# Kernel tuning notes

Measured on AMD Instinct MI355X. Metric: run time of the kernel, lower is better.

Reference implementation:

```python
import jax, jax.numpy as jnp
import numpy as np

D_MODEL = 1024
BATCH = 16
SEQ = 1024
RATIO = 2.0 / 3.0  # layer_idx=2, n_layers=4
THRESH = 0.5


def _layer_norm(x, gamma, beta, eps=1e-5):
    mu = jnp.mean(x, axis=-1, keepdims=True)
    var = jnp.var(x, axis=-1, keepdims=True)
    return (x - mu) * jax.lax.rsqrt(var + eps) * gamma + beta


def _ternary(x):
    # FixedThresholdTernarySpike(threshold=0.5): sign(x) if |x|>0.5 else 0
    return jnp.where(x > THRESH, 1.0, jnp.where(x < -THRESH, -1.0, 0.0)).astype(x.dtype)


def setup_inputs() -> dict:
    key = jax.random.key(0)
    ks = jax.random.split(key, 10)
    scale = 0.1 / np.sqrt(D_MODEL)
    x = jax.random.normal(ks[0], (BATCH, SEQ, D_MODEL), dtype=jnp.float32)
    S0 = jnp.zeros((BATCH, D_MODEL), dtype=jnp.float32)
    mix_init = 1.0 - RATIO
    return {
        "x": x,
        "S0": S0,
        "ln_gamma": jnp.ones((D_MODEL,), jnp.float32),
        "ln_beta": jnp.zeros((D_MODEL,), jnp.float32),
        "time_mix_k": jnp.full((D_MODEL,), mix_init, jnp.float32) + 0.02 * jax.random.normal(ks[1], (D_MODEL,)),
        "time_mix_v": jnp.full((D_MODEL,), mix_init, jnp.float32) + 0.02 * jax.random.normal(ks[2], (D_MODEL,)),
        "time_mix_r": jnp.full((D_MODEL,), mix_init, jnp.float32) + 0.02 * jax.random.normal(ks[3], (D_MODEL,)),
        "decay_weight": jnp.full((D_MODEL,), -0.5, jnp.float32) + 0.02 * jax.random.normal(ks[4], (D_MODEL,)),
        "Wk": scale * jax.random.normal(ks[5], (D_MODEL, D_MODEL), jnp.float32),
        "Wv": scale * jax.random.normal(ks[6], (D_MODEL, D_MODEL), jnp.float32),
        "Wr": scale * jax.random.normal(ks[7], (D_MODEL, D_MODEL), jnp.float32),
        "Wo": scale * jax.random.normal(ks[8], (D_MODEL, D_MODEL), jnp.float32),
    }


def reference(x, S0, ln_gamma, ln_beta, time_mix_k, time_mix_v, time_mix_r,
              decay_weight, Wk, Wv, Wr, Wo):
    # x: (B, T, D)
    x_norm = _layer_norm(x, ln_gamma, ln_beta)                       # LN applied to every step
    # prev_x at t is LN(x[t-1]); at t=0 it is zeros (module uses zeros_like, not LN of zeros)
    prev_norm = jnp.concatenate([jnp.zeros_like(x_norm[:, :1]), x_norm[:, :-1]], axis=1)

    xk = x_norm * time_mix_k + prev_norm * (1.0 - time_mix_k)
    xv = x_norm * time_mix_v + prev_norm * (1.0 - time_mix_v)
    xr = x_norm * time_mix_r + prev_norm * (1.0 - time_mix_r)

    k = _ternary(jnp.einsum('btd,ed->bte', xk, Wk))                  # ternary spikes
    v = _ternary(jnp.einsum('btd,ed->bte', xv, Wv))
    r = jax.nn.sigmoid(jnp.einsum('btd,ed->bte', xr, Wr))

    decay = jax.nn.sigmoid(decay_weight)                             # (D,)
    kv = k * v                                                       # (B, T, D)

    def step(S, kv_t):                                               # S: (B, D)
        S_new = decay * S + kv_t
        return S_new, S_new

    S_final, S_all = jax.lax.scan(step, S0, jnp.swapaxes(kv, 0, 1))  # S_all: (T, B, D)
    S_all = jnp.swapaxes(S_all, 0, 1)                                # (B, T, D)

    out = x + r * jnp.einsum('btd,ed->bte', S_all, Wo)
    return out, S_final
```

## Files before the change

kernel.cpp:

```cpp
#include <hip/hip_runtime.h>
#include <hip/hip_bf16.h>
#include <math.h>

#define D_MODEL 1024
#define SEQ 1024
#define BATCH 16
#define NROWS (BATCH * SEQ)
#define KT8 8

typedef float f32x4 __attribute__((ext_vector_type(4)));
typedef int   i32x4 __attribute__((ext_vector_type(4)));
typedef int   i32x8 __attribute__((ext_vector_type(8)));
typedef __hip_bfloat16 bf16;
typedef unsigned char u8;

__device__ __forceinline__ float bf2f(bf16 v) { return __bfloat162float(v); }
__device__ __forceinline__ bf16 f2bf(float v) { return __float2bfloat16(v); }

__device__ __forceinline__ void gload_lds16(const u8* g, u8* l) {
    __builtin_amdgcn_global_load_lds(
        (const __attribute__((address_space(1))) void*)g,
        (__attribute__((address_space(3))) void*)l, 16, 0, 0);
}

__device__ __forceinline__ int pk_fp8x4(float a, float b, float c, float d) {
    int r = __builtin_amdgcn_cvt_pk_fp8_f32(a, b, 0, false);
    r = __builtin_amdgcn_cvt_pk_fp8_f32(c, d, r, true);
    return r;
}

__device__ __forceinline__ void tile_coords128(int lin, int& m0, int& n0) {
    const int xcd = lin & 7;
    const int loc = lin >> 3;
    m0 = (xcd * 16 + (loc & 15)) * 128;
    n0 = (loc >> 4) * 128;
}

__global__ void conv_w4_kernel(const float* __restrict__ s0, const float* __restrict__ s1,
                               const float* __restrict__ s2, const float* __restrict__ s3,
                               u8* __restrict__ dst) {
    const float* srcs[4] = {s0, s1, s2, s3};
    const float* src = srcs[blockIdx.y];
    int* d = reinterpret_cast<int*>(dst + (size_t)blockIdx.y * (D_MODEL * D_MODEL));
    int i = blockIdx.x * blockDim.x + threadIdx.x;
    const int stride = gridDim.x * blockDim.x;
    for (; i < (D_MODEL * D_MODEL) / 4; i += stride) {
        float4 f = reinterpret_cast<const float4*>(src)[i];
        d[i] = pk_fp8x4(f.x, f.y, f.z, f.w);
    }
}

__global__ __launch_bounds__(256) void lnmix_kernel(
    const float* __restrict__ x, const float* __restrict__ gamma, const float* __restrict__ beta,
    const float* __restrict__ tmk, const float* __restrict__ tmv, const float* __restrict__ tmr,
    u8* __restrict__ xk, u8* __restrict__ xv, u8* __restrict__ xr)
{
    const int wave = threadIdx.x >> 6, lane = threadIdx.x & 63;
    const int lb = (blockIdx.x & 7) * (gridDim.x >> 3) + (blockIdx.x >> 3);
    const int row = lb * 4 + wave;
    const int t = row & (SEQ - 1);
    const size_t base = (size_t)row * D_MODEL;

    float4 vc[4], vp[4];
    float sc = 0.f, sc2 = 0.f, sp = 0.f, sp2 = 0.f;
#pragma unroll
    for (int c = 0; c < 4; c++) {
        const int d = lane * 4 + c * 256;
        vc[c] = *reinterpret_cast<const float4*>(x + base + d);
        if (t == 0) { vp[c] = make_float4(0.f, 0.f, 0.f, 0.f); }
        else        { vp[c] = *reinterpret_cast<const float4*>(x + base - D_MODEL + d); }
        sc  += vc[c].x + vc[c].y + vc[c].z + vc[c].w;
        sc2 += vc[c].x * vc[c].x + vc[c].y * vc[c].y + vc[c].z * vc[c].z + vc[c].w * vc[c].w;
        sp  += vp[c].x + vp[c].y + vp[c].z + vp[c].w;
        sp2 += vp[c].x * vp[c].x + vp[c].y * vp[c].y + vp[c].z * vp[c].z + vp[c].w * vp[c].w;
    }
#pragma unroll
    for (int off = 1; off < 64; off <<= 1) {
        sc  += __shfl_xor(sc, off);
        sc2 += __shfl_xor(sc2, off);
        sp  += __shfl_xor(sp, off);
        sp2 += __shfl_xor(sp2, off);
    }
    const float muc = sc * (1.0f / D_MODEL);
    const float rc  = rsqrtf(sc2 * (1.0f / D_MODEL) - muc * muc + 1e-5f);
    const float mup = sp * (1.0f / D_MODEL);
    const float rp  = rsqrtf(sp2 * (1.0f / D_MODEL) - mup * mup + 1e-5f);

#pragma unroll
    for (int c = 0; c < 4; c++) {
        const int d = lane * 4 + c * 256;
        float4 g  = *reinterpret_cast<const float4*>(gamma + d);
        float4 b  = *reinterpret_cast<const float4*>(beta + d);
        float4 mk = *reinterpret_cast<const float4*>(tmk + d);
        float4 mv = *reinterpret_cast<const float4*>(tmv + d);
        float4 mr = *reinterpret_cast<const float4*>(tmr + d);
        float cn[4], pn[4];
        cn[0] = (vc[c].x - muc) * rc * g.x + b.x;
        cn[1] = (vc[c].y - muc) * rc * g.y + b.y;
        cn[2] = (vc[c].z - muc) * rc * g.z + b.z;
        cn[3] = (vc[c].w - muc) * rc * g.w + b.w;
        if (t == 0) { pn[0] = pn[1] = pn[2] = pn[3] = 0.f; }
        else {
            pn[0] = (vp[c].x - mup) * rp * g.x + b.x;
            pn[1] = (vp[c].y - mup) * rp * g.y + b.y;
            pn[2] = (vp[c].z - mup) * rp * g.z + b.z;
            pn[3] = (vp[c].w - mup) * rp * g.w + b.w;
        }
        const float mkv[4] = {mk.x, mk.y, mk.z, mk.w};
        const float mvv[4] = {mv.x, mv.y, mv.z, mv.w};
        const float mrv[4] = {mr.x, mr.y, mr.z, mr.w};
        float ok[4], ov[4], orr[4];
#pragma unroll
        for (int e = 0; e < 4; e++) {
            ok[e]  = mkv[e] * cn[e] + (1.0f - mkv[e]) * pn[e];
            ov[e]  = mvv[e] * cn[e] + (1.0f - mvv[e]) * pn[e];
            orr[e] = mrv[e] * cn[e] + (1.0f - mrv[e]) * pn[e];
        }
        *reinterpret_cast<int*>(xk + base + d) = pk_fp8x4(ok[0], ok[1], ok[2], ok[3]);
        *reinterpret_cast<int*>(xv + base + d) = pk_fp8x4(ov[0], ov[1], ov[2], ov[3]);
        *reinterpret_cast<int*>(xr + base + d) = pk_fp8x4(orr[0], orr[1], orr[2], orr[3]);
    }
}

__device__ __forceinline__ void gemm128_fp8_dual(
    const u8* __restrict__ A0, const u8* __restrict__ W0,
    const u8* __restrict__ A1, const u8* __restrict__ W1,
    u8* __restrict__ lds,
    int m0, int n0, f32x4 (&acc0)[4][4], f32x4 (&acc1)[4][4])
{
    const int tid  = threadIdx.x;
    const int wave = tid >> 6, lane = tid & 63;
    const int wm = wave >> 1, wn = wave & 1;
    const int mf = lane & 15, quad = lane >> 4;
    const int srow = tid >> 3;
    const int u  = (tid & 7) ^ (srow & 7);
    const int sw = (((u & 3) << 1) | (u >> 2)) * 16;

    const u8* A0g = A0 + (size_t)(m0 + srow) * D_MODEL + sw;
    const u8* B0g = W0 + (size_t)(n0 + srow) * D_MODEL + sw;
    const u8* A1g = A1 + (size_t)(m0 + srow) * D_MODEL + sw;
    const u8* B1g = W1 + (size_t)(n0 + srow) * D_MODEL + sw;

    u8* As0 = lds;
    u8* Bs0 = lds + 16384;
    u8* As1 = lds + 32768;
    u8* Bs1 = lds + 49152;

    const int swz0 = ((quad)     ^ (mf & 7)) * 16;
    const int swz1 = ((4 + quad) ^ (mf & 7)) * 16;
    const int aRow = (wm * 64 + mf) * 128;
    const int bRow = (wn * 64 + mf) * 128;

#pragma unroll 1
    for (int kt = 0; kt < KT8; ++kt) {
        __syncthreads();
#pragma unroll
        for (int g = 0; g < 4; ++g) {
            const size_t go = (size_t)g * 32 * D_MODEL + kt * 128;
            const int lo = g * 4096 + wave * 1024;
            gload_lds16(A0g + go, As0 + lo);
            gload_lds16(B0g + go, Bs0 + lo);
            gload_lds16(A1g + go, As1 + lo);
            gload_lds16(B1g + go, Bs1 + lo);
        }
        __syncthreads();

        i32x8 af[4], bf[4];
#pragma unroll
        for (int i = 0; i < 4; ++i) {
            i32x4 lo = *reinterpret_cast<const i32x4*>(As0 + aRow + i * 2048 + swz0);
            i32x4 hi = *reinterpret_cast<const i32x4*>(As0 + aRow + i * 2048 + swz1);
            af[i] = __builtin_shufflevector(lo, hi, 0, 1, 2, 3, 4, 5, 6, 7);
        }
#pragma unroll
        for (int j = 0; j < 4; ++j) {
            i32x4 lo = *reinterpret_cast<const i32x4*>(Bs0 + bRow + j * 2048 + swz0);
            i32x4 hi = *reinterpret_cast<const i32x4*>(Bs0 + bRow + j * 2048 + swz1);
            bf[j] = __builtin_shufflevector(lo, hi, 0, 1, 2, 3, 4, 5, 6, 7);
        }
#pragma unroll
        for (int i = 0; i < 4; ++i)
#pragma unroll
            for (int j = 0; j < 4; ++j)
                acc0[i][j] = __builtin_amdgcn_mfma_scale_f32_16x16x128_f8f6f4(
                    af[i], bf[j], acc0[i][j], 0, 0, 0, 127, 0, 127);
#pragma unroll
        for (int i = 0; i < 4; ++i) {
            i32x4 lo = *reinterpret_cast<const i32x4*>(As1 + aRow + i * 2048 + swz0);
            i32x4 hi = *reinterpret_cast<const i32x4*>(As1 + aRow + i * 2048 + swz1);
            af[i] = __builtin_shufflevector(lo, hi, 0, 1, 2, 3, 4, 5, 6, 7);
        }
#pragma unroll
        for (int j = 0; j < 4; ++j) {
            i32x4 lo = *reinterpret_cast<const i32x4*>(Bs1 + bRow + j * 2048 + swz0);
            i32x4 hi = *reinterpret_cast<const i32x4*>(Bs1 + bRow + j * 2048 + swz1);
            bf[j] = __builtin_shufflevector(lo, hi, 0, 1, 2, 3, 4, 5, 6, 7);
        }
#pragma unroll
        for (int i = 0; i < 4; ++i)
#pragma unroll
            for (int j = 0; j < 4; ++j)
                acc1[i][j] = __builtin_amdgcn_mfma_scale_f32_16x16x128_f8f6f4(
                    af[i], bf[j], acc1[i][j], 0, 0, 0, 127, 0, 127);
    }
}

__global__ __launch_bounds__(256, 2) void gemm128_kv(
    const u8* __restrict__ XK, const u8* __restrict__ Wk,
    const u8* __restrict__ XV, const u8* __restrict__ Wv,
    char* __restrict__ OK, char* __restrict__ OV)
{
    __shared__ __align__(16) u8 lds[65536];
    int m0, n0;
    tile_coords128(blockIdx.x, m0, n0);

    f32x4 acc0[4][4] = {}, acc1[4][4] = {};
    gemm128_fp8_dual(XK, Wk, XV, Wv, lds, m0, n0, acc0, acc1);

    const int lane = threadIdx.x & 63, wave = threadIdx.x >> 6;
    const int wm = wave >> 1, wn = wave & 1;
    const int mf = lane & 15, quad = lane >> 4;
#pragma unroll
    for (int i = 0; i < 4; ++i)
#pragma unroll
        for (int j = 0; j < 4; ++j)
#pragma unroll
            for (int e = 0; e < 4; ++e) {
                const int row = m0 + wm * 64 + i * 16 + quad * 4 + e;
                const int col = n0 + wn * 64 + j * 16 + mf;
                const size_t o = (size_t)row * D_MODEL + col;
                const float k = acc0[i][j][e];
                const float v = acc1[i][j][e];
                OK[o] = (k > 0.5f) ? 1 : ((k < -0.5f) ? -1 : 0);
                OV[o] = (v > 0.5f) ? 1 : ((v < -0.5f) ? -1 : 0);
            }
}

__global__ __launch_bounds__(512) void scan_kernel(
    const char* __restrict__ K8, const char* __restrict__ V8,
    const float* __restrict__ dw, const float* __restrict__ S0,
    u8* __restrict__ sall, float* __restrict__ sfinal)
{
    __shared__ unsigned int kvp[8][8][64];
    __shared__ float Lf[8][64];
    __shared__ float P[8][64];

    const int bid = blockIdx.x;
    const int db  = bid & 15, b = bid >> 4;
    const int ch  = threadIdx.x & 63;
    const int q   = threadIdx.x >> 6;
    const int d   = db * 64 + ch;

    const float dec = 1.0f / (1.0f + __expf(-dw[d]));
    float c128 = dec;
#pragma unroll
    for (int i = 0; i < 7; i++) c128 *= c128;

    const size_t base = ((size_t)b * SEQ + q * 128) * D_MODEL + d;

    float S = 0.f;
    size_t idx = base;
    unsigned int w = 0;
    for (int t = 0; t < 128; t += 4, idx += 4 * D_MODEL) {
        const int k0 = K8[idx];
        const int v0 = V8[idx];
        const int k1 = K8[idx + 1 * D_MODEL];
        const int v1 = V8[idx + 1 * D_MODEL];
        const int k2 = K8[idx + 2 * D_MODEL];
        const int v2 = V8[idx + 2 * D_MODEL];
        const int k3 = K8[idx + 3 * D_MODEL];
        const int v3 = V8[idx + 3 * D_MODEL];
        const int p0 = k0 * v0, p1 = k1 * v1, p2 = k2 * v2, p3 = k3 * v3;
        S = dec * S + (float)p0;
        S = dec * S + (float)p1;
        S = dec * S + (float)p2;
        S = dec * S + (float)p3;
        const int sh = 2 * (t & 15);
        w |= ((unsigned int)(p0 + 1) << sh) | ((unsigned int)(p1 + 1) << (sh + 2)) |
             ((unsigned int)(p2 + 1) << (sh + 4)) | ((unsigned int)(p3 + 1) << (sh + 6));
        if ((t & 15) == 12) { kvp[q][t >> 4][ch] = w; w = 0; }
    }

    Lf[q][ch] = S;
    __syncthreads();
    if (q == 0) {
        float p = S0[b * D_MODEL + d];
        P[0][ch] = p;
#pragma unroll
        for (int j = 1; j < 8; ++j) {
            p = Lf[j - 1][ch] + c128 * p;
            P[j][ch] = p;
        }
        p = Lf[7][ch] + c128 * p;
        sfinal[b * D_MODEL + d] = p;
    }
    __syncthreads();

    float Sv = P[q][ch];
    idx = base;
    for (int t16 = 0; t16 < 8; ++t16) {
        const unsigned int pw = kvp[q][t16][ch];
#pragma unroll
        for (int j = 0; j < 16; ++j, idx += D_MODEL) {
            const float p = (float)((int)((pw >> (2 * j)) & 3) - 1);
            Sv = dec * Sv + p;
            const int enc = __builtin_amdgcn_cvt_pk_fp8_f32(Sv, 0.f, 0, false);
            sall[idx] = (u8)(enc & 255);
        }
    }
}

__global__ __launch_bounds__(256, 2) void gemm128_outR(
    const u8* __restrict__ XR, const u8* __restrict__ Wr,
    const u8* __restrict__ SA, const u8* __restrict__ Wo,
    const float* __restrict__ x, float* __restrict__ out)
{
    __shared__ __align__(16) u8 lds[65536];
    int m0, n0;
    tile_coords128(blockIdx.x, m0, n0);

    f32x4 accR[4][4] = {}, acc[4][4] = {};
    gemm128_fp8_dual(XR, Wr, SA, Wo, lds, m0, n0, accR, acc);

    const int lane = threadIdx.x & 63, wave = threadIdx.x >> 6;
    const int wm = wave >> 1, wn = wave & 1;
    const int mf = lane & 15, quad = lane >> 4;
#pragma unroll
    for (int i = 0; i < 4; ++i)
#pragma unroll
        for (int j = 0; j < 4; ++j)
#pragma unroll
            for (int e = 0; e < 4; ++e) {
                const int row = m0 + wm * 64 + i * 16 + quad * 4 + e;
                const int col = n0 + wn * 64 + j * 16 + mf;
                const size_t o = (size_t)row * D_MODEL + col;
                const float r = 1.0f / (1.0f + __expf(-accR[i][j][e]));
                out[o] = x[o] + r * acc[i][j][e];
            }
}

extern "C" void kernel_launch(void* const* d_in, const int* in_sizes, int n_in,
                              void* d_out, int out_size, void* d_ws, size_t ws_size,
                              hipStream_t stream) {
    const float* x     = (const float*)d_in[0];
    const float* S0    = (const float*)d_in[1];
    const float* gamma = (const float*)d_in[2];
    const float* beta  = (const float*)d_in[3];
    const float* tmk   = (const float*)d_in[4];
    const float* tmv   = (const float*)d_in[5];
    const float* tmr   = (const float*)d_in[6];
    const float* dw    = (const float*)d_in[7];
    const float* Wk    = (const float*)d_in[8];
    const float* Wv    = (const float*)d_in[9];
    const float* Wr    = (const float*)d_in[10];
    const float* Wo    = (const float*)d_in[11];
    float* out = (float*)d_out;

    const int WN = D_MODEL * D_MODEL;
    const size_t MATN = (size_t)NROWS * D_MODEL;

    u8* ws   = (u8*)d_ws;
    u8* Wk8  = ws;
    u8* Wv8  = Wk8 + WN;
    u8* Wr8  = Wv8 + WN;
    u8* Wo8  = Wr8 + WN;
    u8* XK8  = Wo8 + WN;
    u8* XV8  = XK8 + MATN;
    u8* XR8  = XV8 + MATN;
    char* Kt8 = (char*)(XR8 + MATN);
    char* Vt8 = Kt8 + MATN;
    u8* SA8  = (u8*)(Vt8 + MATN);

    conv_w4_kernel<<<dim3(256, 4), 256, 0, stream>>>(Wk, Wv, Wr, Wo, ws);

    lnmix_kernel<<<NROWS / 4, 256, 0, stream>>>(x, gamma, beta, tmk, tmv, tmr, XK8, XV8, XR8);

    gemm128_kv<<<1024, 256, 0, stream>>>(XK8, Wk8, XV8, Wv8, Kt8, Vt8);

    scan_kernel<<<256, 512, 0, stream>>>(Kt8, Vt8, dw, S0, SA8, out + MATN);

    gemm128_outR<<<1024, 256, 0, stream>>>(XR8, Wr8, SA8, Wo8, x, out);
}
```

Before: 268.6 us.

## Reuse LN rows in lnmix, fuse k*v product, prefetch residual in output GEMM

```diff
diff --git a/kernel.cpp b/kernel.cpp
--- a/kernel.cpp
+++ b/kernel.cpp
@@ -57,76 +57,95 @@
 {
     const int wave = threadIdx.x >> 6, lane = threadIdx.x & 63;
     const int lb = (blockIdx.x & 7) * (gridDim.x >> 3) + (blockIdx.x >> 3);
-    const int row = lb * 4 + wave;
-    const int t = row & (SEQ - 1);
-    const size_t base = (size_t)row * D_MODEL;
-
-    float4 vc[4], vp[4];
-    float sc = 0.f, sc2 = 0.f, sp = 0.f, sp2 = 0.f;
+    const int row0 = (lb * 4 + wave) * 4;
+    const int t0 = row0 & (SEQ - 1);
+
+    float4 g[4], b[4], mk[4], mv[4], mr[4];
 #pragma unroll
     for (int c = 0; c < 4; c++) {
         const int d = lane * 4 + c * 256;
-        vc[c] = *reinterpret_cast<const float4*>(x + base + d);
-        if (t == 0) { vp[c] = make_float4(0.f, 0.f, 0.f, 0.f); }
-        else        { vp[c] = *reinterpret_cast<const float4*>(x + base - D_MODEL + d); }
-        sc  += vc[c].x + vc[c].y + vc[c].z + vc[c].w;
-        sc2 += vc[c].x * vc[c].x + vc[c].y * vc[c].y + vc[c].z * vc[c].z + vc[c].w * vc[c].w;
-        sp  += vp[c].x + vp[c].y + vp[c].z + vp[c].w;
-        sp2 += vp[c].x * vp[c].x + vp[c].y * vp[c].y + vp[c].z * vp[c].z + vp[c].w * vp[c].w;
-    }
-#pragma unroll
-    for (int off = 1; off < 64; off <<= 1) {
-        sc  += __shfl_xor(sc, off);
-        sc2 += __shfl_xor(sc2, off);
-        sp  += __shfl_xor(sp, off);
-        sp2 += __shfl_xor(sp2, off);
-    }
-    const float muc = sc * (1.0f / D_MODEL);
-    const float rc  = rsqrtf(sc2 * (1.0f / D_MODEL) - muc * muc + 1e-5f);
-    const float mup = sp * (1.0f / D_MODEL);
-    const float rp  = rsqrtf(sp2 * (1.0f / D_MODEL) - mup * mup + 1e-5f);
-
-#pragma unroll
-    for (int c = 0; c < 4; c++) {
-        const int d = lane * 4 + c * 256;
-        float4 g  = *reinterpret_cast<const float4*>(gamma + d);
-        float4 b  = *reinterpret_cast<const float4*>(beta + d);
-        float4 mk = *reinterpret_cast<const float4*>(tmk + d);
-        float4 mv = *reinterpret_cast<const float4*>(tmv + d);
-        float4 mr = *reinterpret_cast<const float4*>(tmr + d);
-        float cn[4], pn[4];
-        cn[0] = (vc[c].x - muc) * rc * g.x + b.x;
-        cn[1] = (vc[c].y - muc) * rc * g.y + b.y;
-        cn[2] = (vc[c].z - muc) * rc * g.z + b.z;
-        cn[3] = (vc[c].w - muc) * rc * g.w + b.w;
-        if (t == 0) { pn[0] = pn[1] = pn[2] = pn[3] = 0.f; }
-        else {
-            pn[0] = (vp[c].x - mup) * rp * g.x + b.x;
-            pn[1] = (vp[c].y - mup) * rp * g.y + b.y;
-            pn[2] = (vp[c].z - mup) * rp * g.z + b.z;
-            pn[3] = (vp[c].w - mup) * rp * g.w + b.w;
-        }
-        const float mkv[4] = {mk.x, mk.y, mk.z, mk.w};
-        const float mvv[4] = {mv.x, mv.y, mv.z, mv.w};
-        const float mrv[4] = {mr.x, mr.y, mr.z, mr.w};
-        float ok[4], ov[4], orr[4];
-#pragma unroll
-        for (int e = 0; e < 4; e++) {
-            ok[e]  = mkv[e] * cn[e] + (1.0f - mkv[e]) * pn[e];
-            ov[e]  = mvv[e] * cn[e] + (1.0f - mvv[e]) * pn[e];
-            orr[e] = mrv[e] * cn[e] + (1.0f - mrv[e]) * pn[e];
-        }
-        *reinterpret_cast<int*>(xk + base + d) = pk_fp8x4(ok[0], ok[1], ok[2], ok[3]);
-        *reinterpret_cast<int*>(xv + base + d) = pk_fp8x4(ov[0], ov[1], ov[2], ov[3]);
-        *reinterpret_cast<int*>(xr + base + d) = pk_fp8x4(orr[0], orr[1], orr[2], orr[3]);
-    }
-}
-
+        g[c]  = *reinterpret_cast<const float4*>(gamma + d);
+        b[c]  = *reinterpret_cast<const float4*>(beta + d);
+        mk[c] = *reinterpret_cast<const float4*>(tmk + d);
+        mv[c] = *reinterpret_cast<const float4*>(tmv + d);
+        mr[c] = *reinterpret_cast<const float4*>(tmr + d);
+    }
+
+    float4 pcn[4];
+    if (t0 == 0) {
+#pragma unroll
+        for (int c = 0; c < 4; c++) pcn[c] = make_float4(0.f, 0.f, 0.f, 0.f);
+    } else {
+        const size_t pb = (size_t)(row0 - 1) * D_MODEL;
+        float4 vp[4];
+        float s = 0.f, s2 = 0.f;
+#pragma unroll
+        for (int c = 0; c < 4; c++) {
+            vp[c] = *reinterpret_cast<const float4*>(x + pb + lane * 4 + c * 256);
+            s  += vp[c].x + vp[c].y + vp[c].z + vp[c].w;
+            s2 += vp[c].x * vp[c].x + vp[c].y * vp[c].y + vp[c].z * vp[c].z + vp[c].w * vp[c].w;
+        }
+#pragma unroll
+        for (int off = 1; off < 64; off <<= 1) { s += __shfl_xor(s, off); s2 += __shfl_xor(s2, off); }
+        const float mu = s * (1.0f / D_MODEL);
+        const float rs = rsqrtf(s2 * (1.0f / D_MODEL) - mu * mu + 1e-5f);
+#pragma unroll
+        for (int c = 0; c < 4; c++) {
+            pcn[c].x = (vp[c].x - mu) * rs * g[c].x + b[c].x;
+            pcn[c].y = (vp[c].y - mu) * rs * g[c].y + b[c].y;
+            pcn[c].z = (vp[c].z - mu) * rs * g[c].z + b[c].z;
+            pcn[c].w = (vp[c].w - mu) * rs * g[c].w + b[c].w;
+        }
+    }
+
+#pragma unroll 1
+    for (int r = 0; r < 4; ++r) {
+        const size_t base = (size_t)(row0 + r) * D_MODEL;
+        float4 vc[4];
+        float s = 0.f, s2 = 0.f;
+#pragma unroll
+        for (int c = 0; c < 4; c++) {
+            vc[c] = *reinterpret_cast<const float4*>(x + base + lane * 4 + c * 256);
+            s  += vc[c].x + vc[c].y + vc[c].z + vc[c].w;
+            s2 += vc[c].x * vc[c].x + vc[c].y * vc[c].y + vc[c].z * vc[c].z + vc[c].w * vc[c].w;
+        }
+#pragma unroll
+        for (int off = 1; off < 64; off <<= 1) { s += __shfl_xor(s, off); s2 += __shfl_xor(s2, off); }
+        const float mu = s * (1.0f / D_MODEL);
+        const float rs = rsqrtf(s2 * (1.0f / D_MODEL) - mu * mu + 1e-5f);
+#pragma unroll
+        for (int c = 0; c < 4; c++) {
+            const int d = lane * 4 + c * 256;
+            float cn[4], pn[4], kk[4], vv[4], rr[4];
+            cn[0] = (vc[c].x - mu) * rs * g[c].x + b[c].x;
+            cn[1] = (vc[c].y - mu) * rs * g[c].y + b[c].y;
+            cn[2] = (vc[c].z - mu) * rs * g[c].z + b[c].z;
+            cn[3] = (vc[c].w - mu) * rs * g[c].w + b[c].w;
+            pn[0] = pcn[c].x; pn[1] = pcn[c].y; pn[2] = pcn[c].z; pn[3] = pcn[c].w;
+            const float mkv[4] = {mk[c].x, mk[c].y, mk[c].z, mk[c].w};
+            const float mvv[4] = {mv[c].x, mv[c].y, mv[c].z, mv[c].w};
+            const float mrv[4] = {mr[c].x, mr[c].y, mr[c].z, mr[c].w};
+#pragma unroll
+            for (int e = 0; e < 4; e++) {
+                kk[e] = mkv[e] * cn[e] + (1.0f - mkv[e]) * pn[e];
+                vv[e] = mvv[e] * cn[e] + (1.0f - mvv[e]) * pn[e];
+                rr[e] = mrv[e] * cn[e] + (1.0f - mrv[e]) * pn[e];
+            }
+            *reinterpret_cast<int*>(xk + base + d) = pk_fp8x4(kk[0], kk[1], kk[2], kk[3]);
+            *reinterpret_cast<int*>(xv + base + d) = pk_fp8x4(vv[0], vv[1], vv[2], vv[3]);
+            *reinterpret_cast<int*>(xr + base + d) = pk_fp8x4(rr[0], rr[1], rr[2], rr[3]);
+            pcn[c].x = cn[0]; pcn[c].y = cn[1]; pcn[c].z = cn[2]; pcn[c].w = cn[3];
+        }
+    }
+}
+
+template <bool PFX>
 __device__ __forceinline__ void gemm128_fp8_dual(
     const u8* __restrict__ A0, const u8* __restrict__ W0,
     const u8* __restrict__ A1, const u8* __restrict__ W1,
-    u8* __restrict__ lds,
-    int m0, int n0, f32x4 (&acc0)[4][4], f32x4 (&acc1)[4][4])
+    u8* __restrict__ lds, int m0, int n0,
+    f32x4 (&acc0)[4][4], f32x4 (&acc1)[4][4],
+    const float* __restrict__ xg, float* xr_)
 {
     const int tid  = threadIdx.x;
     const int wave = tid >> 6, lane = tid & 63;
@@ -163,6 +182,20 @@
             gload_lds16(A1g + go, As1 + lo);
             gload_lds16(B1g + go, Bs1 + lo);
         }
+        if (PFX && (kt == 4 || kt == 5)) {
+            const int i0 = (kt == 4) ? 0 : 2;
+#pragma unroll
+            for (int i = 0; i < 2; ++i)
+#pragma unroll
+                for (int j = 0; j < 4; ++j)
+#pragma unroll
+                    for (int e = 0; e < 4; ++e) {
+                        const int row = m0 + wm * 64 + (i0 + i) * 16 + quad * 4 + e;
+                        const int col = n0 + wn * 64 + j * 16 + mf;
+                        xr_[(i0 + i) * 16 + j * 4 + e] = xg[(size_t)row * D_MODEL + col];
+                    }
+            asm volatile("" ::: "memory");
+        }
         __syncthreads();
 
         i32x8 af[4], bf[4];
@@ -208,14 +241,14 @@
 __global__ __launch_bounds__(256, 2) void gemm128_kv(
     const u8* __restrict__ XK, const u8* __restrict__ Wk,
     const u8* __restrict__ XV, const u8* __restrict__ Wv,
-    char* __restrict__ OK, char* __restrict__ OV)
+    char* __restrict__ OP)
 {
     __shared__ __align__(16) u8 lds[65536];
     int m0, n0;
     tile_coords128(blockIdx.x, m0, n0);
 
     f32x4 acc0[4][4] = {}, acc1[4][4] = {};
-    gemm128_fp8_dual(XK, Wk, XV, Wv, lds, m0, n0, acc0, acc1);
+    gemm128_fp8_dual<false>(XK, Wk, XV, Wv, lds, m0, n0, acc0, acc1, nullptr, nullptr);
 
     const int lane = threadIdx.x & 63, wave = threadIdx.x >> 6;
     const int wm = wave >> 1, wn = wave & 1;
@@ -228,16 +261,16 @@
             for (int e = 0; e < 4; ++e) {
                 const int row = m0 + wm * 64 + i * 16 + quad * 4 + e;
                 const int col = n0 + wn * 64 + j * 16 + mf;
-                const size_t o = (size_t)row * D_MODEL + col;
                 const float k = acc0[i][j][e];
                 const float v = acc1[i][j][e];
-                OK[o] = (k > 0.5f) ? 1 : ((k < -0.5f) ? -1 : 0);
-                OV[o] = (v > 0.5f) ? 1 : ((v < -0.5f) ? -1 : 0);
+                const int tk = (k > 0.5f) ? 1 : ((k < -0.5f) ? -1 : 0);
+                const int tv = (v > 0.5f) ? 1 : ((v < -0.5f) ? -1 : 0);
+                OP[(size_t)row * D_MODEL + col] = (char)(tk * tv);
             }
 }
 
 __global__ __launch_bounds__(512) void scan_kernel(
-    const char* __restrict__ K8, const char* __restrict__ V8,
+    const char* __restrict__ P8,
     const float* __restrict__ dw, const float* __restrict__ S0,
     u8* __restrict__ sall, float* __restrict__ sfinal)
 {
@@ -262,15 +295,10 @@
     size_t idx = base;
     unsigned int w = 0;
     for (int t = 0; t < 128; t += 4, idx += 4 * D_MODEL) {
-        const int k0 = K8[idx];
-        const int v0 = V8[idx];
-        const int k1 = K8[idx + 1 * D_MODEL];
-        const int v1 = V8[idx + 1 * D_MODEL];
-        const int k2 = K8[idx + 2 * D_MODEL];
-        const int v2 = V8[idx + 2 * D_MODEL];
-        const int k3 = K8[idx + 3 * D_MODEL];
-        const int v3 = V8[idx + 3 * D_MODEL];
-        const int p0 = k0 * v0, p1 = k1 * v1, p2 = k2 * v2, p3 = k3 * v3;
+        const int p0 = P8[idx];
+        const int p1 = P8[idx + 1 * D_MODEL];
+        const int p2 = P8[idx + 2 * D_MODEL];
+        const int p3 = P8[idx + 3 * D_MODEL];
         S = dec * S + (float)p0;
         S = dec * S + (float)p1;
         S = dec * S + (float)p2;
@@ -319,8 +347,9 @@
     int m0, n0;
     tile_coords128(blockIdx.x, m0, n0);
 
+    float xr_[64];
     f32x4 accR[4][4] = {}, acc[4][4] = {};
-    gemm128_fp8_dual(XR, Wr, SA, Wo, lds, m0, n0, accR, acc);
+    gemm128_fp8_dual<true>(XR, Wr, SA, Wo, lds, m0, n0, accR, acc, x, xr_);
 
     const int lane = threadIdx.x & 63, wave = threadIdx.x >> 6;
     const int wm = wave >> 1, wn = wave & 1;
@@ -335,7 +364,7 @@
                 const int col = n0 + wn * 64 + j * 16 + mf;
                 const size_t o = (size_t)row * D_MODEL + col;
                 const float r = 1.0f / (1.0f + __expf(-accR[i][j][e]));
-                out[o] = x[o] + r * acc[i][j][e];
+                out[o] = xr_[i * 16 + j * 4 + e] + r * acc[i][j][e];
             }
 }
 
@@ -367,17 +396,16 @@
     u8* XK8  = Wo8 + WN;
     u8* XV8  = XK8 + MATN;
     u8* XR8  = XV8 + MATN;
-    char* Kt8 = (char*)(XR8 + MATN);
-    char* Vt8 = Kt8 + MATN;
-    u8* SA8  = (u8*)(Vt8 + MATN);
+    char* P8 = (char*)(XR8 + MATN);
+    u8* SA8  = (u8*)(P8 + MATN);
 
     conv_w4_kernel<<<dim3(256, 4), 256, 0, stream>>>(Wk, Wv, Wr, Wo, ws);
 
-    lnmix_kernel<<<NROWS / 4, 256, 0, stream>>>(x, gamma, beta, tmk, tmv, tmr, XK8, XV8, XR8);
-
-    gemm128_kv<<<1024, 256, 0, stream>>>(XK8, Wk8, XV8, Wv8, Kt8, Vt8);
-
-    scan_kernel<<<256, 512, 0, stream>>>(Kt8, Vt8, dw, S0, SA8, out + MATN);
+    lnmix_kernel<<<NROWS / 16, 256, 0, stream>>>(x, gamma, beta, tmk, tmv, tmr, XK8, XV8, XR8);
+
+    gemm128_kv<<<1024, 256, 0, stream>>>(XK8, Wk8, XV8, Wv8, P8);
+
+    scan_kernel<<<256, 512, 0, stream>>>(P8, dw, S0, SA8, out + MATN);
 
     gemm128_outR<<<1024, 256, 0, stream>>>(XR8, Wr8, SA8, Wo8, x, out);
 }
```

Measured after the change: 275.0 us. 1.02x slower.
